# Performance work log

Hardware: AMD Instinct MI355X
Metric: run time of the kernel (lower is better)

Reference implementation:

```python
import jax, jax.numpy as jnp
import numpy as np

H = W = 512
A = 256  # number of projection angles


def setup_inputs() -> dict:
    key = jax.random.key(0)
    k1, k2 = jax.random.split(key)
    data = jax.random.normal(k1, (1, 1, H, W), dtype=jnp.float32)
    # angles uniform in [0, pi) -- realistic tomographic scan range
    angles = jax.random.uniform(k2, (A,), dtype=jnp.float32) * np.float32(np.pi)
    return {"data": data, "angles": angles}


def _radon(data, angles):
    B, C, h, w = data.shape  # B == C == 1 structurally required by the torch module
    nA = angles.shape[0]
    cos = jnp.cos(angles)
    sin = jnp.sin(angles)

    # F.affine_grid(align_corners=False) base coordinates: pixel centers in [-1, 1]
    xs = (2.0 * jnp.arange(w, dtype=data.dtype) + 1.0) / w - 1.0  # [W]
    ys = (2.0 * jnp.arange(h, dtype=data.dtype) + 1.0) / h - 1.0  # [H]
    by, bx = jnp.meshgrid(ys, xs, indexing="ij")  # [H,W]

    # theta built from -angles: rows [cos a, sin a, 0; -sin a, cos a, 0]
    gx = cos[:, None, None] * bx + sin[:, None, None] * by  # [A,H,W]
    gy = -sin[:, None, None] * bx + cos[:, None, None] * by  # [A,H,W]

    # grid_sample(align_corners=False): unnormalize to input pixel coords
    ix = ((gx + 1.0) * w - 1.0) * 0.5
    iy = ((gy + 1.0) * h - 1.0) * 0.5

    x0 = jnp.floor(ix).astype(jnp.int32)
    y0 = jnp.floor(iy).astype(jnp.int32)
    x1 = x0 + 1
    y1 = y0 + 1
    wx1 = ix - x0.astype(data.dtype)
    wx0 = 1.0 - wx1
    wy1 = iy - y0.astype(data.dtype)
    wy0 = 1.0 - wy1

    img = data[0, 0]  # [H,W]

    def gather(yy, xx):
        # zero padding: out-of-range taps contribute 0
        valid = (xx >= 0) & (xx < w) & (yy >= 0) & (yy < h)
        v = img[jnp.clip(yy, 0, h - 1), jnp.clip(xx, 0, w - 1)]
        return jnp.where(valid, v, jnp.zeros((), data.dtype))

    rotated = (wy0 * (wx0 * gather(y0, x0) + wx1 * gather(y0, x1))
               + wy1 * (wx0 * gather(y1, x0) + wx1 * gather(y1, x1)))  # [A,H,W]

    proj = jnp.sum(rotated, axis=1)  # sum over height -> [A,W]
    return proj.reshape(1, 1, nA, w)


def reference(data, angles):
    return _radon(data, angles)
```

## Files before the change

### kernel.cpp

```cpp
#include <hip/hip_runtime.h>


#define HH 512
#define WW 512
#define NA 256
#define XC 64
#define NXC (WW / XC)
#define NW 8
#define YC 48
#define NCH 11
#define LASTR 32
#define ROWS_MAX 82
#define SMAX 97
#define PAD 112
#define PW (WW + 2 * PAD)
#define PH (HH + 2 * PAD)

typedef float f32x2 __attribute__((ext_vector_type(2)));

__global__ __launch_bounds__(256) void pad_kernel(
    const float* __restrict__ img, float* __restrict__ P)
{
    const int c = blockIdx.x * 256 + threadIdx.x;
    const int r = blockIdx.y;
    if (c >= PW) return;
    const int gr = r - PAD, gc = c - PAD;
    float v = 0.0f;
    if ((unsigned)gr < (unsigned)HH && (unsigned)gc < (unsigned)WW)
        v = img[gr * WW + gc];
    P[r * PW + c] = v;
}

__device__ __forceinline__ float fract_f(float x) {
#if __has_builtin(__builtin_amdgcn_fractf)
    return __builtin_amdgcn_fractf(x);
#else
    return x - floorf(x);
#endif
}

struct BB {
    int c_lo, r_lo, bh, bw;
    bool valid;
    float v0;
};

template <int STRIDE, int NYS>
__device__ __forceinline__ void sample_chunk(
    const float* __restrict__ tb, const BB& b,
    const float s, const float c, const float u, const int wid,
    float& acc0, float& acc1)
{
    const float bc = fmaf(c, u, 255.5f - (float)b.c_lo);
    const float br = fmaf(-s, u, 255.5f - (float)b.r_lo);
    const float vy0 = b.v0 + (float)(wid * NYS);

    f32x2 crx, stepv;
    crx.x = fmaf(s, vy0, bc);
    crx.y = fmaf(c, vy0, br);
    stepv.x = s;
    stepv.y = c;

#pragma unroll
    for (int i = 0; i < NYS; ++i) {
        const float cxl = crx.x;
        const float rxl = crx.y;
        const int ci = (int)cxl;
        const int ri = (int)rxl;
        const float wx1 = fract_f(cxl);
        const float wy1 = fract_f(rxl);

        __builtin_assume(ri >= 0 && ri < ROWS_MAX);
        __builtin_assume(ci >= 0 && ci < SMAX);
        const int ad = ri * STRIDE + ci;

        f32x2 top, bot;
        top.x = tb[ad];
        top.y = tb[ad + 1];
        bot.x = tb[ad + STRIDE];
        bot.y = tb[ad + STRIDE + 1];

        f32x2 wyv;
        wyv.x = wy1;
        wyv.y = wy1;
        const f32x2 pv = __builtin_elementwise_fma(wyv, bot - top, top);

        acc0 += pv.x;
        acc1 = fmaf(wx1, pv.y - pv.x, acc1);

        crx += stepv;
    }
}

template <bool PADDED, int STRIDE>
__device__ __forceinline__ void radon_body(
    const float* __restrict__ src, float* __restrict__ tile,
    const float s, const float c, const int lane, const int wid, const int x0,
    float& acc0, float& acc1)
{
    constexpr bool CPOS = (STRIDE == 95);

    const float u  = (float)(x0 + lane) + (0.5f - 256.0f);
    const float u0 = (float)x0 + (0.5f - 256.0f);
    const float u1 = u0 + (float)(XC - 1);

    const float* __restrict__ Porg = PADDED ? (src + PAD * PW + PAD) : src;

    auto bbox = [&](int k) -> BB {
        BB b;
        const int rows = (k == NCH - 1) ? LASTR : YC;
        b.v0 = (float)(k * YC) - 255.5f;
        const float v1 = b.v0 + (float)(rows - 1);
        float cx_min, cx_max, rx_min, rx_max;
        if (CPOS) {
            cx_min = fmaf(c, u0, fmaf(s, b.v0, 255.5f));
            cx_max = fmaf(c, u1, fmaf(s, v1,   255.5f));
            rx_min = fmaf(-s, u1, fmaf(c, b.v0, 255.5f));
            rx_max = fmaf(-s, u0, fmaf(c, v1,   255.5f));
        } else {
            cx_min = fmaf(c, u1, fmaf(s, b.v0, 255.5f));
            cx_max = fmaf(c, u0, fmaf(s, v1,   255.5f));
            rx_min = fmaf(-s, u1, fmaf(c, v1,   255.5f));
            rx_max = fmaf(-s, u0, fmaf(c, b.v0, 255.5f));
        }
        b.c_lo = (int)floorf(cx_min);
        b.r_lo = (int)floorf(rx_min);
        const int c_hi = (int)floorf(cx_max) + 1;
        const int r_hi = (int)floorf(rx_max) + 1;
        b.bh = min(r_hi - b.r_lo + 1, ROWS_MAX);
        b.bw = min(c_hi - b.c_lo + 1, SMAX);
        b.valid = (b.c_lo <= WW - 1) & (c_hi >= 0) & (b.r_lo <= HH - 1) & (r_hi >= 0);
        return b;
    };

    auto stage = [&](int buf, const BB& b) {
        float* __restrict__ base = tile + buf * (ROWS_MAX * SMAX);
        if (PADDED) {
            if (lane < 21) {
                const float* g = Porg + (b.r_lo + wid) * PW + b.c_lo + lane * 4;
                float* l = base + wid * STRIDE;
                for (int r = wid; r < b.bh; r += NW) {
                    __builtin_amdgcn_global_load_lds(
                        (__attribute__((address_space(1))) const void*)g,
                        (__attribute__((address_space(3))) void*)l, 16, 0, 0);
                    g += NW * PW;
                    l += NW * STRIDE;
                }
            }
        } else {
            for (int r = wid; r < b.bh; r += NW) {
                const int gr = b.r_lo + r;
                const bool row_ok = ((unsigned)gr < (unsigned)HH);
                const float* __restrict__ rowp = src + gr * WW;
                for (int cc = lane; cc < b.bw; cc += 64) {
                    const int gc = b.c_lo + cc;
                    float v = 0.0f;
                    if (row_ok) {
                        const int gcl = min(max(gc, 0), WW - 1);
                        const float t = rowp[gcl];
                        v = ((unsigned)gc < (unsigned)WW) ? t : 0.0f;
                    }
                    base[r * STRIDE + cc] = v;
                }
            }
        }
    };

    BB cur = bbox(0);
    if (cur.valid) stage(0, cur);

#pragma unroll 1
    for (int k = 0; k < NCH; ++k) {
        BB nxt;
        nxt.valid = false;
        if (k + 1 < NCH) nxt = bbox(k + 1);

        __syncthreads();

        if (nxt.valid) stage((k + 1) & 1, nxt);

        if (cur.valid) {
            const float* tb = tile + (k & 1) * (ROWS_MAX * SMAX);
            if (k == NCH - 1)
                sample_chunk<STRIDE, LASTR / NW>(tb, cur, s, c, u, wid, acc0, acc1);
            else
                sample_chunk<STRIDE, YC / NW>(tb, cur, s, c, u, wid, acc0, acc1);
        }
        cur = nxt;
    }
}

template <bool PADDED>
__global__ __launch_bounds__(512, 4) void radon_kernel(
    const float* __restrict__ src,
    const float* __restrict__ angles, float* __restrict__ out)
{
    __shared__ float tile[2 * ROWS_MAX * SMAX];

    const int tid  = threadIdx.x;
    const int lane = tid & 63;
    const int wid  = tid >> 6;

    const int a  = blockIdx.x >> 3;
    const int x0 = (blockIdx.x & 7) * XC;

    float s, c;
    sincosf(angles[a], &s, &c);

    float acc0 = 0.0f, acc1 = 0.0f;
    if (c >= 0.0f)
        radon_body<PADDED, 95>(src, tile, s, c, lane, wid, x0, acc0, acc1);
    else
        radon_body<PADDED, 97>(src, tile, s, c, lane, wid, x0, acc0, acc1);

    __syncthreads();
    tile[tid] = acc0 + acc1;
    __syncthreads();
    if (tid < 64) {
        float r = tile[tid];
#pragma unroll
        for (int k = 1; k < NW; ++k) r += tile[k * 64 + tid];
        out[a * WW + x0 + tid] = r;
    }
}

extern "C" void kernel_launch(void* const* d_in, const int* in_sizes, int n_in,
                              void* d_out, int out_size, void* d_ws, size_t ws_size,
                              hipStream_t stream) {
    const float* img    = (const float*)d_in[0];
    const float* angles = (const float*)d_in[1];
    float* out = (float*)d_out;
    float* P   = (float*)d_ws;

    const bool padded = (ws_size >= (size_t)PW * PH * sizeof(float));

    if (padded) {
        pad_kernel<<<dim3((PW + 255) / 256, PH), 256, 0, stream>>>(img, P);
        radon_kernel<true><<<dim3(NA * NXC), 512, 0, stream>>>(P, angles, out);
    } else {
        radon_kernel<false><<<dim3(NA * NXC), 512, 0, stream>>>(img, angles, out);
    }
}
```

Before: 126.1 us.

## Stage tiles through registers with single LDS buffer and larger row chunks

Replaces the double-buffered LDS staging (global_load_lds direct-to-LDS) with a register-prefetch pipeline: the next chunk is loaded into registers two steps ahead, then written into a single LDS tile after sampling finishes. Chunk height grows from 48 to 64 rows, which removes the special last chunk, and launch bounds are raised to 8 blocks per CU because the LDS footprint is halved. This aims at more occupancy and better hiding of load latency. The cost is extra VGPR pressure from the prefetch slots and two barriers per chunk.

```diff
diff --git a/kernel.cpp b/kernel.cpp
--- a/kernel.cpp
+++ b/kernel.cpp
@@ -7,16 +7,18 @@
 #define XC 64
 #define NXC (WW / XC)
 #define NW 8
-#define YC 48
-#define NCH 11
-#define LASTR 32
-#define ROWS_MAX 82
+#define YC 64
+#define NCH (HH / YC)
+#define ROWS_MAX 92
 #define SMAX 97
+#define SEGW 23
+#define NSLOT 5
 #define PAD 112
 #define PW (WW + 2 * PAD)
 #define PH (HH + 2 * PAD)
 
 typedef float f32x2 __attribute__((ext_vector_type(2)));
+typedef float f32x4 __attribute__((ext_vector_type(4)));
 
 __global__ __launch_bounds__(256) void pad_kernel(
     const float* __restrict__ img, float* __restrict__ P)
@@ -39,13 +41,19 @@
 #endif
 }
 
+__device__ __forceinline__ f32x4 load4(const float* p) {
+    f32x4 v;
+    __builtin_memcpy(&v, p, 16);
+    return v;
+}
+
 struct BB {
-    int c_lo, r_lo, bh, bw;
+    int c_lo, r_lo, bh;
     bool valid;
     float v0;
 };
 
-template <int STRIDE, int NYS>
+template <int STRIDE>
 __device__ __forceinline__ void sample_chunk(
     const float* __restrict__ tb, const BB& b,
     const float s, const float c, const float u, const int wid,
@@ -53,7 +61,7 @@
 {
     const float bc = fmaf(c, u, 255.5f - (float)b.c_lo);
     const float br = fmaf(-s, u, 255.5f - (float)b.r_lo);
-    const float vy0 = b.v0 + (float)(wid * NYS);
+    const float vy0 = b.v0 + (float)(wid * (YC / NW));
 
     f32x2 crx, stepv;
     crx.x = fmaf(s, vy0, bc);
@@ -62,7 +70,7 @@
     stepv.y = c;
 
 #pragma unroll
-    for (int i = 0; i < NYS; ++i) {
+    for (int i = 0; i < YC / NW; ++i) {
         const float cxl = crx.x;
         const float rxl = crx.y;
         const int ci = (int)cxl;
@@ -96,7 +104,7 @@
 __device__ __forceinline__ void radon_body(
     const float* __restrict__ src, float* __restrict__ tile,
     const float s, const float c, const int lane, const int wid, const int x0,
-    float& acc0, float& acc1)
+    const int tid, float& acc0, float& acc1)
 {
     constexpr bool CPOS = (STRIDE == 95);
 
@@ -108,9 +116,8 @@
 
     auto bbox = [&](int k) -> BB {
         BB b;
-        const int rows = (k == NCH - 1) ? LASTR : YC;
         b.v0 = (float)(k * YC) - 255.5f;
-        const float v1 = b.v0 + (float)(rows - 1);
+        const float v1 = b.v0 + (float)(YC - 1);
         float cx_min, cx_max, rx_min, rx_max;
         if (CPOS) {
             cx_min = fmaf(c, u0, fmaf(s, b.v0, 255.5f));
@@ -128,31 +135,82 @@
         const int c_hi = (int)floorf(cx_max) + 1;
         const int r_hi = (int)floorf(rx_max) + 1;
         b.bh = min(r_hi - b.r_lo + 1, ROWS_MAX);
-        b.bw = min(c_hi - b.c_lo + 1, SMAX);
         b.valid = (b.c_lo <= WW - 1) & (c_hi >= 0) & (b.r_lo <= HH - 1) & (r_hi >= 0);
         return b;
     };
 
-    auto stage = [&](int buf, const BB& b) {
-        float* __restrict__ base = tile + buf * (ROWS_MAX * SMAX);
-        if (PADDED) {
-            if (lane < 21) {
-                const float* g = Porg + (b.r_lo + wid) * PW + b.c_lo + lane * 4;
-                float* l = base + wid * STRIDE;
-                for (int r = wid; r < b.bh; r += NW) {
-                    __builtin_amdgcn_global_load_lds(
-                        (__attribute__((address_space(1))) const void*)g,
-                        (__attribute__((address_space(3))) void*)l, 16, 0, 0);
-                    g += NW * PW;
-                    l += NW * STRIDE;
+    if (PADDED) {
+        f32x4 p[NSLOT];
+
+        auto prefetch = [&](const BB& b) {
+            const float* gb = Porg + b.r_lo * PW + b.c_lo;
+            const int n = b.bh * SEGW;
+#pragma unroll
+            for (int i = 0; i < NSLOT; ++i) {
+                const int e = tid + i * 512;
+                if (e < n) {
+                    const int r = (int)(((unsigned)(e * 2850)) >> 16);
+                    p[i] = load4(gb + 4 * e + (PW - 4 * SEGW) * r);
                 }
             }
-        } else {
+        };
+
+        auto write_tile = [&](const BB& b) {
+            const int n = b.bh * SEGW;
+#pragma unroll
+            for (int i = 0; i < NSLOT; ++i) {
+                const int e = tid + i * 512;
+                if (e < n) {
+                    const int r = (int)(((unsigned)(e * 2850)) >> 16);
+                    const int o = 4 * e + (STRIDE - 4 * SEGW) * r;
+                    tile[o]     = p[i].x;
+                    tile[o + 1] = p[i].y;
+                    tile[o + 2] = p[i].z;
+                    tile[o + 3] = p[i].w;
+                }
+            }
+        };
+
+        BB cur = bbox(0);
+        BB nxt = bbox(1);
+        if (cur.valid) {
+            prefetch(cur);
+            write_tile(cur);
+        }
+        if (nxt.valid) prefetch(nxt);
+        __syncthreads();
+
+#pragma unroll 1
+        for (int k = 0; k < NCH; ++k) {
+            BB n2;
+            n2.valid = false;
+            if (k + 2 < NCH) n2 = bbox(k + 2);
+
+            if (cur.valid)
+                sample_chunk<STRIDE>(tile, cur, s, c, u, wid, acc0, acc1);
+
+            __syncthreads();
+
+            if (nxt.valid) write_tile(nxt);
+            if (n2.valid)  prefetch(n2);
+
+            __syncthreads();
+
+            cur = nxt;
+            nxt = n2;
+        }
+    } else {
+#pragma unroll 1
+        for (int k = 0; k < NCH; ++k) {
+            BB b = bbox(k);
+            if (!b.valid) { __syncthreads(); __syncthreads(); continue; }
+            const int bw = SMAX;
+            __syncthreads();
             for (int r = wid; r < b.bh; r += NW) {
                 const int gr = b.r_lo + r;
                 const bool row_ok = ((unsigned)gr < (unsigned)HH);
                 const float* __restrict__ rowp = src + gr * WW;
-                for (int cc = lane; cc < b.bw; cc += 64) {
+                for (int cc = lane; cc < bw; cc += 64) {
                     const int gc = b.c_lo + cc;
                     float v = 0.0f;
                     if (row_ok) {
@@ -160,42 +218,22 @@
                         const float t = rowp[gcl];
                         v = ((unsigned)gc < (unsigned)WW) ? t : 0.0f;
                     }
-                    base[r * STRIDE + cc] = v;
+                    tile[r * STRIDE + cc] = v;
                 }
             }
-        }
-    };
-
-    BB cur = bbox(0);
-    if (cur.valid) stage(0, cur);
-
-#pragma unroll 1
-    for (int k = 0; k < NCH; ++k) {
-        BB nxt;
-        nxt.valid = false;
-        if (k + 1 < NCH) nxt = bbox(k + 1);
-
+            __syncthreads();
+            sample_chunk<STRIDE>(tile, b, s, c, u, wid, acc0, acc1);
+        }
         __syncthreads();
-
-        if (nxt.valid) stage((k + 1) & 1, nxt);
-
-        if (cur.valid) {
-            const float* tb = tile + (k & 1) * (ROWS_MAX * SMAX);
-            if (k == NCH - 1)
-                sample_chunk<STRIDE, LASTR / NW>(tb, cur, s, c, u, wid, acc0, acc1);
-            else
-                sample_chunk<STRIDE, YC / NW>(tb, cur, s, c, u, wid, acc0, acc1);
-        }
-        cur = nxt;
     }
 }
 
 template <bool PADDED>
-__global__ __launch_bounds__(512, 4) void radon_kernel(
+__global__ __launch_bounds__(512, 8) void radon_kernel(
     const float* __restrict__ src,
     const float* __restrict__ angles, float* __restrict__ out)
 {
-    __shared__ float tile[2 * ROWS_MAX * SMAX];
+    __shared__ float tile[ROWS_MAX * SMAX];
 
     const int tid  = threadIdx.x;
     const int lane = tid & 63;
@@ -209,9 +247,9 @@
 
     float acc0 = 0.0f, acc1 = 0.0f;
     if (c >= 0.0f)
-        radon_body<PADDED, 95>(src, tile, s, c, lane, wid, x0, acc0, acc1);
+        radon_body<PADDED, 95>(src, tile, s, c, lane, wid, x0, tid, acc0, acc1);
     else
-        radon_body<PADDED, 97>(src, tile, s, c, lane, wid, x0, acc0, acc1);
+        radon_body<PADDED, 97>(src, tile, s, c, lane, wid, x0, tid, acc0, acc1);
 
     __syncthreads();
     tile[tid] = acc0 + acc1;
```

New measurement: 148.6 us. 1.18x slower.
